# Kernel tuning notes

Measured on AMD Instinct MI355X. Metric: run time of the kernel, lower is better.

Reference implementation:

```python
import math
import jax, jax.numpy as jnp
import numpy as np

WH, WW = 8, 8
NUM_HEADS = 4
EMBED_DIMS = 128
N_TOK = WH * WW

# --- static relative position index (N, N) ---
_coords = np.stack(np.meshgrid(np.arange(WH), np.arange(WW), indexing='ij')).reshape(2, -1)
_rel = (_coords[:, :, None] - _coords[:, None, :]).transpose(1, 2, 0).copy()
_rel[..., 0] += WH - 1
_rel[..., 1] += WW - 1
_rel[..., 0] *= 2 * WW - 1
REL_INDEX = _rel.sum(-1)  # (N, N) ints in [0, (2Wh-1)(2Ww-1))

# --- static log-spaced relative coords table ((2Wh-1)*(2Ww-1), 2) ---
_ch = np.arange(-(WH - 1), WH, dtype=np.float32)
_cw = np.arange(-(WW - 1), WW, dtype=np.float32)
_tab = np.stack(np.meshgrid(_ch, _cw, indexing='ij')).reshape(2, -1).T.copy()
_tab[:, 0] /= WH - 1
_tab[:, 1] /= WW - 1
_tab *= 8
COORDS_TABLE = np.sign(_tab) * np.log2(np.abs(_tab) + 1.0) / math.log2(8)  # (225, 2)


def setup_inputs() -> dict:
    key = jax.random.key(0)
    ks = jax.random.split(key, 8)
    B_ = 8192
    C = EMBED_DIMS
    H = NUM_HEADS
    return {
        'x': jax.random.normal(ks[0], (B_, N_TOK, C), dtype=jnp.float32),
        'mask': jnp.zeros((256, N_TOK, N_TOK), dtype=jnp.float32),
        'qkv_w': jax.random.normal(ks[1], (3 * C, C), dtype=jnp.float32) * 0.02,
        'q_bias': jnp.zeros((C,), dtype=jnp.float32),
        'v_bias': jnp.zeros((C,), dtype=jnp.float32),
        'logit_scale': jnp.full((H, 1, 1), math.log(10.0), dtype=jnp.float32),
        'cpb_w1': jax.random.normal(ks[2], (512, 2), dtype=jnp.float32) * 0.02,
        'cpb_b1': jnp.zeros((512,), dtype=jnp.float32),
        'cpb_w2': jax.random.normal(ks[3], (H, 512), dtype=jnp.float32) * 0.02,
        'proj_w': jax.random.normal(ks[4], (C, C), dtype=jnp.float32) * 0.02,
        'proj_b': jnp.zeros((C,), dtype=jnp.float32),
    }


def reference(x, mask, qkv_w, q_bias, v_bias, logit_scale, cpb_w1, cpb_b1, cpb_w2, proj_w, proj_b):
    B_, N, C = x.shape
    H = NUM_HEADS
    D = C // H
    # qkv with q/v bias only (k bias is zero)
    qkv_b = jnp.concatenate([q_bias, jnp.zeros_like(v_bias), v_bias])
    qkv = x @ qkv_w.T + qkv_b                           # (B_, N, 3C)
    qkv = qkv.reshape(B_, N, 3, H, D).transpose(2, 0, 3, 1, 4)
    q, k, v = qkv[0], qkv[1], qkv[2]                    # (B_, H, N, D)
    # cosine attention
    qn = q / jnp.clip(jnp.linalg.norm(q, axis=-1, keepdims=True), 1e-12)
    kn = k / jnp.clip(jnp.linalg.norm(k, axis=-1, keepdims=True), 1e-12)
    attn = jnp.einsum('bhnd,bhmd->bhnm', qn, kn)
    scale = jnp.exp(jnp.minimum(logit_scale, math.log(1.0 / 0.01)))  # (H,1,1)
    attn = attn * scale
    # log-CPB relative position bias
    table = jnp.asarray(COORDS_TABLE, dtype=x.dtype)     # (225, 2)
    hdn = jax.nn.relu(table @ cpb_w1.T + cpb_b1)         # (225, 512)
    bias_table = hdn @ cpb_w2.T                          # (225, H)
    rel_idx = jnp.asarray(REL_INDEX.reshape(-1))
    bias = bias_table[rel_idx].reshape(N, N, H).transpose(2, 0, 1)
    bias = 16.0 * jax.nn.sigmoid(bias)                   # (H, N, N)
    attn = attn + bias[None]
    # shifted-window mask
    nW = mask.shape[0]
    attn = attn.reshape(B_ // nW, nW, H, N, N) + mask[None, :, None]
    attn = jax.nn.softmax(attn.reshape(B_, H, N, N), axis=-1)
    out = jnp.einsum('bhnm,bhmd->bhnd', attn, v)
    out = out.transpose(0, 2, 1, 3).reshape(B_, N, C)
    return out @ proj_w.T + proj_b
```

## Files before the change

### kernel.cpp

```cpp
#include <hip/hip_runtime.h>

typedef __attribute__((ext_vector_type(8))) __bf16 bf16x8;
typedef __attribute__((ext_vector_type(4))) float floatx4;

#define WS_BIAS  131072
#define WS_SCALE 196608
#define WS_TBL   196640
#define WS_ETAB  262144

static __device__ __forceinline__ unsigned short f2bf_u(float f) {
  union { __bf16 b; unsigned short u; } cv; cv.b = (__bf16)f; return cv.u;
}
static __device__ __forceinline__ unsigned pkbf(float lo, float hi) {
  union { __bf16 b[2]; unsigned u; } cv; cv.b[0] = (__bf16)lo; cv.b[1] = (__bf16)hi; return cv.u;
}
static __device__ __forceinline__ float bfu_lo(unsigned u) { return __uint_as_float(u << 16); }
static __device__ __forceinline__ float bfu_hi(unsigned u) { return __uint_as_float(u & 0xffff0000u); }

__global__ void k_prep_weights(const float* __restrict__ qkv_w,
                               const float* __restrict__ proj_w,
                               const float* __restrict__ logit_scale,
                               unsigned short* __restrict__ wsQ,
                               float* __restrict__ wsScale)
{
  int t = blockIdx.x * 256 + threadIdx.x;
  int i4 = t * 4;
  float4 v;
  if (i4 < 49152) v = *reinterpret_cast<const float4*>(qkv_w + i4);
  else            v = *reinterpret_cast<const float4*>(proj_w + (i4 - 49152));
  ushort4 pk;
  pk.x = f2bf_u(v.x); pk.y = f2bf_u(v.y); pk.z = f2bf_u(v.z); pk.w = f2bf_u(v.w);
  *reinterpret_cast<ushort4*>(wsQ + i4) = pk;
  if (t < 4) wsScale[t] = expf(fminf(logit_scale[t], 4.6051702f));
}

__global__ void k_cpb_table(const float* __restrict__ w1, const float* __restrict__ b1,
                            const float* __restrict__ w2, float* __restrict__ tbl)
{
  __shared__ float red[256][4];
  int t = blockIdx.x;
  int i = t / 15, j = t % 15;
  float c0 = 8.f * (float)(i - 7) / 7.f;
  float c1 = 8.f * (float)(j - 7) / 7.f;
  c0 = copysignf(log2f(fabsf(c0) + 1.f) / 3.f, c0);
  c1 = copysignf(log2f(fabsf(c1) + 1.f) / 3.f, c1);
  float a0 = 0.f, a1 = 0.f, a2 = 0.f, a3 = 0.f;
  for (int k = threadIdx.x; k < 512; k += 256) {
    float hd = fmaxf(c0 * w1[2*k] + c1 * w1[2*k+1] + b1[k], 0.f);
    a0 += hd * w2[k]; a1 += hd * w2[512+k]; a2 += hd * w2[1024+k]; a3 += hd * w2[1536+k];
  }
  red[threadIdx.x][0]=a0; red[threadIdx.x][1]=a1; red[threadIdx.x][2]=a2; red[threadIdx.x][3]=a3;
  __syncthreads();
  for (int s = 128; s > 0; s >>= 1) {
    if (threadIdx.x < (unsigned)s) {
      red[threadIdx.x][0] += red[threadIdx.x+s][0];
      red[threadIdx.x][1] += red[threadIdx.x+s][1];
      red[threadIdx.x][2] += red[threadIdx.x+s][2];
      red[threadIdx.x][3] += red[threadIdx.x+s][3];
    }
    __syncthreads();
  }
  if (threadIdx.x < 4) tbl[t*4 + threadIdx.x] = red[0][threadIdx.x];
}

__global__ void k_cpb_bias(const float* __restrict__ tbl, float* __restrict__ biasT)
{
  int idx = blockIdx.x * 256 + threadIdx.x;
  int hh = idx >> 12, n = (idx >> 6) & 63, m = idx & 63;
  int rel = ((n >> 3) - (m >> 3) + 7) * 15 + ((n & 7) - (m & 7) + 7);
  float bv = tbl[rel * 4 + hh];
  biasT[idx] = 16.f / (1.f + expf(-bv));
}

__global__ void k_exp_table(const float* __restrict__ biasT, const float* __restrict__ mask,
                            unsigned short* __restrict__ E)
{
  int idx4 = (blockIdx.x * 256 + threadIdx.x) * 4;
  int wm  = idx4 >> 14;
  int rem = idx4 & 16383;
  int hh  = rem >> 12;
  int nm  = rem & 4095;
  float4 mv = *reinterpret_cast<const float4*>(mask + (wm << 12) + nm);
  float4 bv = *reinterpret_cast<const float4*>(biasT + (hh << 12) + nm);
  ushort4 o;
  o.x = f2bf_u(expf(bv.x + mv.x));
  o.y = f2bf_u(expf(bv.y + mv.y));
  o.z = f2bf_u(expf(bv.z + mv.z));
  o.w = f2bf_u(expf(bv.w + mv.w));
  *reinterpret_cast<ushort4*>(E + idx4) = o;
}

__global__ __launch_bounds__(256, 2) void k_wmsa(
    const float* __restrict__ x,
    const unsigned short* __restrict__ wqkv, const unsigned short* __restrict__ wproj,
    const float* __restrict__ q_bias, const float* __restrict__ v_bias,
    const unsigned short* __restrict__ Etab, const float* __restrict__ scale4,
    const float* __restrict__ proj_b, float* __restrict__ out)
{
  __shared__ char s_x[64 * 256];
  __shared__ char s_qk[4][8192];
  __shared__ char s_vT[4][4096];

  const int blk  = blockIdx.x;
  const int tid  = threadIdx.x;
  const int lane = tid & 63;
  const int h    = tid >> 6;
  const int l15  = lane & 15;
  const int lh   = lane >> 4;
  const int swq  = ((l15 ^ (l15 >> 2)) & 3) << 4;
  const int swp  = (l15 & 7) << 4;
  const floatx4 zf4 = {0.f, 0.f, 0.f, 0.f};

  bf16x8 wvf[4][2], wff[4][4];
  #pragma unroll
  for (int kk = 0; kk < 4; ++kk) {
    #pragma unroll
    for (int ft = 0; ft < 2; ++ft)
      wvf[kk][ft] = *reinterpret_cast<const bf16x8*>(
          wqkv + (size_t)(256 + h * 32 + ft * 16 + l15) * 128 + kk * 32 + lh * 8);
    #pragma unroll
    for (int ff = 0; ff < 4; ++ff) {
      int fb = (ff < 2) ? (h * 32 + ff * 16) : (128 + h * 32 + (ff - 2) * 16);
      wff[kk][ff] = *reinterpret_cast<const bf16x8*>(
          wqkv + (size_t)(fb + l15) * 128 + kk * 32 + lh * 8);
    }
  }
  floatx4 qb0 = *reinterpret_cast<const floatx4*>(q_bias + h * 32 + lh * 4);
  floatx4 qb1 = *reinterpret_cast<const floatx4*>(q_bias + h * 32 + 16 + lh * 4);
  const float vb0 = v_bias[h * 32 + l15], vb1 = v_bias[h * 32 + 16 + l15];
  const float sc  = scale4[h] * 1.44269504f;
  const unsigned short* Eh = Etab + ((size_t)((blk & 255) * 4 + h)) * 4096;

  float4 xpre[8];

  #pragma unroll
  for (int wi = 0; wi < 2; ++wi) {
    const size_t b = (size_t)blk + (size_t)wi * 4096;

    if (wi) __syncthreads();

    {
      int r = tid >> 2;
      if (wi == 0) {
        const float* xb = x + b * 8192;
        #pragma unroll
        for (int cc = 0; cc < 8; ++cc) {
          int c = (tid & 3) + cc * 4;
          float4 v = reinterpret_cast<const float4*>(xb)[r * 32 + c];
          uint2 w; w.x = pkbf(v.x, v.y); w.y = pkbf(v.z, v.w);
          *reinterpret_cast<uint2*>(s_x + r * 256 + ((c * 8) ^ ((r & 7) << 4))) = w;
        }
      } else {
        #pragma unroll
        for (int cc = 0; cc < 8; ++cc) {
          int c = (tid & 3) + cc * 4;
          uint2 w; w.x = pkbf(xpre[cc].x, xpre[cc].y); w.y = pkbf(xpre[cc].z, xpre[cc].w);
          *reinterpret_cast<uint2*>(s_x + r * 256 + ((c * 8) ^ ((r & 7) << 4))) = w;
        }
      }
    }
    __syncthreads();

    floatx4 vacc[4][2];
    floatx4 qk[4][4];
    #pragma unroll
    for (int mt = 0; mt < 4; ++mt) { vacc[mt][0] = zf4; vacc[mt][1] = zf4; }
    #pragma unroll
    for (int ff = 0; ff < 4; ++ff)
      #pragma unroll
      for (int tt = 0; tt < 4; ++tt) qk[ff][tt] = zf4;

    #pragma unroll
    for (int kk = 0; kk < 4; ++kk) {
      bf16x8 xf[4];
      #pragma unroll
      for (int tt = 0; tt < 4; ++tt) {
        int row = tt * 16 + l15;
        xf[tt] = *reinterpret_cast<const bf16x8*>(
            s_x + row * 256 + (((kk * 32 + lh * 8) * 2) ^ ((row & 7) << 4)));
      }
      #pragma unroll
      for (int ft = 0; ft < 2; ++ft)
        #pragma unroll
        for (int mt = 0; mt < 4; ++mt)
          vacc[mt][ft] = __builtin_amdgcn_mfma_f32_16x16x32_bf16(xf[mt], wvf[kk][ft], vacc[mt][ft], 0, 0, 0);
      #pragma unroll
      for (int ff = 0; ff < 4; ++ff)
        #pragma unroll
        for (int tt = 0; tt < 4; ++tt)
          qk[ff][tt] = __builtin_amdgcn_mfma_f32_16x16x32_bf16(wff[kk][ff], xf[tt], qk[ff][tt], 0, 0, 0);
    }

    {
      char* sv = s_vT[h];
      #pragma unroll
      for (int mt = 0; mt < 4; ++mt) {
        #pragma unroll
        for (int ft = 0; ft < 2; ++ft) {
          float vb = ft ? vb1 : vb0;
          int d = ft * 16 + l15;
          uint2 w;
          w.x = pkbf(vacc[mt][ft][0] + vb, vacc[mt][ft][1] + vb);
          w.y = pkbf(vacc[mt][ft][2] + vb, vacc[mt][ft][3] + vb);
          *reinterpret_cast<uint2*>(sv + d * 128 + (((mt * 16 + lh * 4) * 2) ^ swp)) = w;
        }
      }
    }

    #pragma unroll
    for (int tt = 0; tt < 4; ++tt)
      #pragma unroll
      for (int r = 0; r < 4; ++r) { qk[0][tt][r] += qb0[r]; qk[1][tt][r] += qb1[r]; }
    #pragma unroll
    for (int tt = 0; tt < 4; ++tt) {
      float sq = 0.f, sk = 0.f;
      #pragma unroll
      for (int r = 0; r < 4; ++r) {
        sq += qk[0][tt][r] * qk[0][tt][r] + qk[1][tt][r] * qk[1][tt][r];
        sk += qk[2][tt][r] * qk[2][tt][r] + qk[3][tt][r] * qk[3][tt][r];
      }
      sq += __shfl_xor(sq, 16); sq += __shfl_xor(sq, 32);
      sk += __shfl_xor(sk, 16); sk += __shfl_xor(sk, 32);
      float rq = sc  / fmaxf(sqrtf(sq), 1e-12f);
      float rk = 1.f / fmaxf(sqrtf(sk), 1e-12f);
      #pragma unroll
      for (int r = 0; r < 4; ++r) {
        qk[0][tt][r] *= rq; qk[1][tt][r] *= rq;
        qk[2][tt][r] *= rk; qk[3][tt][r] *= rk;
      }
    }

    uint2 e[4][4];
    #pragma unroll
    for (int tn = 0; tn < 4; ++tn)
      #pragma unroll
      for (int tm = 0; tm < 4; ++tm)
        e[tn][tm] = *reinterpret_cast<const uint2*>(
            Eh + (tn * 16 + l15) * 64 + tm * 16 + lh * 4);

    {
      char* sq = s_qk[h];
      #pragma unroll
      for (int tt = 0; tt < 4; ++tt) {
        int row = 16 * tt + l15;
        #pragma unroll
        for (int ff = 0; ff < 2; ++ff) {
          uint2 wq_, wk_;
          wq_.x = pkbf(qk[ff][tt][0],     qk[ff][tt][1]);
          wq_.y = pkbf(qk[ff][tt][2],     qk[ff][tt][3]);
          wk_.x = pkbf(qk[2 + ff][tt][0], qk[2 + ff][tt][1]);
          wk_.y = pkbf(qk[2 + ff][tt][2], qk[2 + ff][tt][3]);
          int colb = (ff * 32 + lh * 8) ^ swq;
          *reinterpret_cast<uint2*>(sq + row * 64 + colb)        = wq_;
          *reinterpret_cast<uint2*>(sq + 4096 + row * 64 + colb) = wk_;
        }
      }
    }

    floatx4 rs;
    {
      const char* sq = s_qk[h];
      bf16x8 qf[4], kf[4];
      #pragma unroll
      for (int tt = 0; tt < 4; ++tt) {
        int row = 16 * tt + l15;
        qf[tt] = *reinterpret_cast<const bf16x8*>(sq + row * 64 + ((lh * 16) ^ swq));
        kf[tt] = *reinterpret_cast<const bf16x8*>(sq + 4096 + row * 64 + ((lh * 16) ^ swq));
      }
      char* sp = s_qk[h];

      #pragma unroll
      for (int tn = 0; tn < 4; ++tn) {
        floatx4 sacc[4];
        #pragma unroll
        for (int tm = 0; tm < 4; ++tm)
          sacc[tm] = __builtin_amdgcn_mfma_f32_16x16x32_bf16(kf[tm], qf[tn], zf4, 0, 0, 0);
        float sum = 0.f;
        uint2 pw[4];
        #pragma unroll
        for (int tm = 0; tm < 4; ++tm) {
          uint2 eu = e[tn][tm];
          float e0 = exp2f(sacc[tm][0]) * bfu_lo(eu.x);
          float e1 = exp2f(sacc[tm][1]) * bfu_hi(eu.x);
          float e2 = exp2f(sacc[tm][2]) * bfu_lo(eu.y);
          float e3 = exp2f(sacc[tm][3]) * bfu_hi(eu.y);
          sum += (e0 + e1) + (e2 + e3);
          pw[tm].x = pkbf(e0, e1); pw[tm].y = pkbf(e2, e3);
        }
        sum += __shfl_xor(sum, 16); sum += __shfl_xor(sum, 32);
        rs[tn] = 1.f / sum;
        int prow = 16 * tn + l15;
        #pragma unroll
        for (int tm = 0; tm < 4; ++tm)
          *reinterpret_cast<uint2*>(sp + prow * 128 + ((tm * 32 + lh * 8) ^ swp)) = pw[tm];
      }
    }

    bf16x8 wp[4][2];
    #pragma unroll
    for (int kk = 0; kk < 4; ++kk)
      #pragma unroll
      for (int ft = 0; ft < 2; ++ft)
        wp[kk][ft] = *reinterpret_cast<const bf16x8*>(
            wproj + (size_t)(h * 32 + ft * 16 + l15) * 128 + kk * 32 + lh * 8);
    if (wi == 0) {
      const float* xb1 = x + ((size_t)blk + 4096) * 8192;
      int r = tid >> 2;
      #pragma unroll
      for (int cc = 0; cc < 8; ++cc) {
        int c = (tid & 3) + cc * 4;
        xpre[cc] = reinterpret_cast<const float4*>(xb1)[r * 32 + c];
      }
    }

    floatx4 oacc[2][4];
    #pragma unroll
    for (int dt = 0; dt < 2; ++dt)
      #pragma unroll
      for (int nt = 0; nt < 4; ++nt) oacc[dt][nt] = zf4;
    {
      const char* sv = s_vT[h];
      const char* sp = s_qk[h];
      #pragma unroll
      for (int kk = 0; kk < 2; ++kk) {
        bf16x8 vf[2];
        #pragma unroll
        for (int dt = 0; dt < 2; ++dt)
          vf[dt] = *reinterpret_cast<const bf16x8*>(
              sv + (dt * 16 + l15) * 128 + ((kk * 64 + lh * 16) ^ swp));
        #pragma unroll
        for (int nt = 0; nt < 4; ++nt) {
          bf16x8 pf = *reinterpret_cast<const bf16x8*>(
              sp + (nt * 16 + l15) * 128 + ((kk * 64 + lh * 16) ^ swp));
          #pragma unroll
          for (int dt = 0; dt < 2; ++dt)
            oacc[dt][nt] = __builtin_amdgcn_mfma_f32_16x16x32_bf16(vf[dt], pf, oacc[dt][nt], 0, 0, 0);
        }
      }
    }
    __syncthreads();

    #pragma unroll
    for (int dt = 0; dt < 2; ++dt) {
      #pragma unroll
      for (int nt = 0; nt < 4; ++nt) {
        int n = nt * 16 + l15;
        uint2 w;
        w.x = pkbf(oacc[dt][nt][0] * rs[nt], oacc[dt][nt][1] * rs[nt]);
        w.y = pkbf(oacc[dt][nt][2] * rs[nt], oacc[dt][nt][3] * rs[nt]);
        *reinterpret_cast<uint2*>(
            s_x + n * 256 + (((h * 32 + dt * 16 + lh * 4) * 2) ^ ((n & 7) << 4))) = w;
      }
    }
    __syncthreads();

    floatx4 pacc[4][2];
    #pragma unroll
    for (int mt = 0; mt < 4; ++mt) { pacc[mt][0] = zf4; pacc[mt][1] = zf4; }
    #pragma unroll
    for (int kk = 0; kk < 4; ++kk) {
      bf16x8 of[4];
      #pragma unroll
      for (int mt = 0; mt < 4; ++mt) {
        int row = mt * 16 + l15;
        of[mt] = *reinterpret_cast<const bf16x8*>(
            s_x + row * 256 + (((kk * 32 + lh * 8) * 2) ^ ((row & 7) << 4)));
      }
      #pragma unroll
      for (int ft = 0; ft < 2; ++ft)
        #pragma unroll
        for (int mt = 0; mt < 4; ++mt)
          pacc[mt][ft] = __builtin_amdgcn_mfma_f32_16x16x32_bf16(of[mt], wp[kk][ft], pacc[mt][ft], 0, 0, 0);
    }
    {
      float pb0 = proj_b[h * 32 + l15], pb1 = proj_b[h * 32 + 16 + l15];
      float* ob = out + b * 8192;
      #pragma unroll
      for (int mt = 0; mt < 4; ++mt)
        #pragma unroll
        for (int r = 0; r < 4; ++r) {
          int n = mt * 16 + lh * 4 + r;
          ob[n * 128 + h * 32 + l15]      = pacc[mt][0][r] + pb0;
          ob[n * 128 + h * 32 + 16 + l15] = pacc[mt][1][r] + pb1;
        }
    }
  }
}

extern "C" void kernel_launch(void* const* d_in, const int* in_sizes, int n_in,
                              void* d_out, int out_size, void* d_ws, size_t ws_size,
                              hipStream_t stream)
{
  const float* x    = (const float*)d_in[0];
  const float* mask = (const float*)d_in[1];
  const float* qkvw = (const float*)d_in[2];
  const float* qb   = (const float*)d_in[3];
  const float* vb   = (const float*)d_in[4];
  const float* ls   = (const float*)d_in[5];
  const float* w1   = (const float*)d_in[6];
  const float* b1   = (const float*)d_in[7];
  const float* w2   = (const float*)d_in[8];
  const float* pw   = (const float*)d_in[9];
  const float* pb   = (const float*)d_in[10];
  float* out = (float*)d_out;
  char* ws = (char*)d_ws;

  unsigned short* wsQ = (unsigned short*)ws;
  float* wsBias  = (float*)(ws + WS_BIAS);
  float* wsScale = (float*)(ws + WS_SCALE);
  float* wsTbl   = (float*)(ws + WS_TBL);
  unsigned short* wsE = (unsigned short*)(ws + WS_ETAB);

  hipLaunchKernelGGL(k_prep_weights, dim3(64), dim3(256), 0, stream, qkvw, pw, ls, wsQ, wsScale);
  hipLaunchKernelGGL(k_cpb_table, dim3(225), dim3(256), 0, stream, w1, b1, w2, wsTbl);
  hipLaunchKernelGGL(k_cpb_bias, dim3(64), dim3(256), 0, stream, wsTbl, wsBias);
  hipLaunchKernelGGL(k_exp_table, dim3(4096), dim3(256), 0, stream, wsBias, mask, wsE);
  hipLaunchKernelGGL(k_wmsa, dim3(4096), dim3(256), 0, stream, x,
                     wsQ, wsQ + 49152, qb, vb, wsE, wsScale, pb, out);
}
```

Before: 289.6 us.

## Split QKV projection into phased V/Q/K passes to cut register pressure

The kernel no longer holds all QKV weight fragments in registers for both windows. It reloads V, Q and K weights from global memory in separate phases, computing each projection and normalizing it before moving on. The software prefetch of the second window's x is dropped, and the exp-bias table is loaded once before the window loop. The aim is to lower live VGPR count and raise occupancy, at the cost of reloading weights each window, reading the x tile from LDS three times, and losing the prefetch overlap.

```diff
diff --git a/kernel.cpp b/kernel.cpp
--- a/kernel.cpp
+++ b/kernel.cpp
@@ -111,27 +111,20 @@
   const int swp  = (l15 & 7) << 4;
   const floatx4 zf4 = {0.f, 0.f, 0.f, 0.f};
 
-  bf16x8 wvf[4][2], wff[4][4];
-  #pragma unroll
-  for (int kk = 0; kk < 4; ++kk) {
-    #pragma unroll
-    for (int ft = 0; ft < 2; ++ft)
-      wvf[kk][ft] = *reinterpret_cast<const bf16x8*>(
-          wqkv + (size_t)(256 + h * 32 + ft * 16 + l15) * 128 + kk * 32 + lh * 8);
-    #pragma unroll
-    for (int ff = 0; ff < 4; ++ff) {
-      int fb = (ff < 2) ? (h * 32 + ff * 16) : (128 + h * 32 + (ff - 2) * 16);
-      wff[kk][ff] = *reinterpret_cast<const bf16x8*>(
-          wqkv + (size_t)(fb + l15) * 128 + kk * 32 + lh * 8);
-    }
-  }
   floatx4 qb0 = *reinterpret_cast<const floatx4*>(q_bias + h * 32 + lh * 4);
   floatx4 qb1 = *reinterpret_cast<const floatx4*>(q_bias + h * 32 + 16 + lh * 4);
   const float vb0 = v_bias[h * 32 + l15], vb1 = v_bias[h * 32 + 16 + l15];
   const float sc  = scale4[h] * 1.44269504f;
+  const float pb0 = proj_b[h * 32 + l15], pb1 = proj_b[h * 32 + 16 + l15];
   const unsigned short* Eh = Etab + ((size_t)((blk & 255) * 4 + h)) * 4096;
 
-  float4 xpre[8];
+  uint2 e[4][4];
+  #pragma unroll
+  for (int tn = 0; tn < 4; ++tn)
+    #pragma unroll
+    for (int tm = 0; tm < 4; ++tm)
+      e[tn][tm] = *reinterpret_cast<const uint2*>(
+          Eh + (tn * 16 + l15) * 64 + tm * 16 + lh * 4);
 
   #pragma unroll
   for (int wi = 0; wi < 2; ++wi) {
@@ -140,58 +133,44 @@
     if (wi) __syncthreads();
 
     {
+      const float* xb = x + b * 8192;
       int r = tid >> 2;
-      if (wi == 0) {
-        const float* xb = x + b * 8192;
-        #pragma unroll
-        for (int cc = 0; cc < 8; ++cc) {
-          int c = (tid & 3) + cc * 4;
-          float4 v = reinterpret_cast<const float4*>(xb)[r * 32 + c];
-          uint2 w; w.x = pkbf(v.x, v.y); w.y = pkbf(v.z, v.w);
-          *reinterpret_cast<uint2*>(s_x + r * 256 + ((c * 8) ^ ((r & 7) << 4))) = w;
-        }
-      } else {
-        #pragma unroll
-        for (int cc = 0; cc < 8; ++cc) {
-          int c = (tid & 3) + cc * 4;
-          uint2 w; w.x = pkbf(xpre[cc].x, xpre[cc].y); w.y = pkbf(xpre[cc].z, xpre[cc].w);
-          *reinterpret_cast<uint2*>(s_x + r * 256 + ((c * 8) ^ ((r & 7) << 4))) = w;
-        }
+      #pragma unroll
+      for (int cc = 0; cc < 8; ++cc) {
+        int c = (tid & 3) + cc * 4;
+        float4 v = reinterpret_cast<const float4*>(xb)[r * 32 + c];
+        uint2 w; w.x = pkbf(v.x, v.y); w.y = pkbf(v.z, v.w);
+        *reinterpret_cast<uint2*>(s_x + r * 256 + ((c * 8) ^ ((r & 7) << 4))) = w;
       }
     }
     __syncthreads();
 
-    floatx4 vacc[4][2];
-    floatx4 qk[4][4];
-    #pragma unroll
-    for (int mt = 0; mt < 4; ++mt) { vacc[mt][0] = zf4; vacc[mt][1] = zf4; }
-    #pragma unroll
-    for (int ff = 0; ff < 4; ++ff)
-      #pragma unroll
-      for (int tt = 0; tt < 4; ++tt) qk[ff][tt] = zf4;
-
-    #pragma unroll
-    for (int kk = 0; kk < 4; ++kk) {
-      bf16x8 xf[4];
-      #pragma unroll
-      for (int tt = 0; tt < 4; ++tt) {
-        int row = tt * 16 + l15;
-        xf[tt] = *reinterpret_cast<const bf16x8*>(
-            s_x + row * 256 + (((kk * 32 + lh * 8) * 2) ^ ((row & 7) << 4)));
-      }
-      #pragma unroll
-      for (int ft = 0; ft < 2; ++ft)
-        #pragma unroll
-        for (int mt = 0; mt < 4; ++mt)
-          vacc[mt][ft] = __builtin_amdgcn_mfma_f32_16x16x32_bf16(xf[mt], wvf[kk][ft], vacc[mt][ft], 0, 0, 0);
-      #pragma unroll
-      for (int ff = 0; ff < 4; ++ff)
-        #pragma unroll
-        for (int tt = 0; tt < 4; ++tt)
-          qk[ff][tt] = __builtin_amdgcn_mfma_f32_16x16x32_bf16(wff[kk][ff], xf[tt], qk[ff][tt], 0, 0, 0);
-    }
-
-    {
+    {
+      bf16x8 wv[4][2];
+      #pragma unroll
+      for (int kk = 0; kk < 4; ++kk)
+        #pragma unroll
+        for (int ft = 0; ft < 2; ++ft)
+          wv[kk][ft] = *reinterpret_cast<const bf16x8*>(
+              wqkv + (size_t)(256 + h * 32 + ft * 16 + l15) * 128 + kk * 32 + lh * 8);
+      floatx4 vacc[4][2];
+      #pragma unroll
+      for (int mt = 0; mt < 4; ++mt) { vacc[mt][0] = zf4; vacc[mt][1] = zf4; }
+      #pragma unroll
+      for (int kk = 0; kk < 4; ++kk) {
+        bf16x8 xf[4];
+        #pragma unroll
+        for (int tt = 0; tt < 4; ++tt) {
+          int row = tt * 16 + l15;
+          xf[tt] = *reinterpret_cast<const bf16x8*>(
+              s_x + row * 256 + (((kk * 32 + lh * 8) * 2) ^ ((row & 7) << 4)));
+        }
+        #pragma unroll
+        for (int ft = 0; ft < 2; ++ft)
+          #pragma unroll
+          for (int mt = 0; mt < 4; ++mt)
+            vacc[mt][ft] = __builtin_amdgcn_mfma_f32_16x16x32_bf16(xf[mt], wv[kk][ft], vacc[mt][ft], 0, 0, 0);
+      }
       char* sv = s_vT[h];
       #pragma unroll
       for (int mt = 0; mt < 4; ++mt) {
@@ -207,68 +186,125 @@
       }
     }
 
-    #pragma unroll
-    for (int tt = 0; tt < 4; ++tt)
-      #pragma unroll
-      for (int r = 0; r < 4; ++r) { qk[0][tt][r] += qb0[r]; qk[1][tt][r] += qb1[r]; }
-    #pragma unroll
-    for (int tt = 0; tt < 4; ++tt) {
-      float sq = 0.f, sk = 0.f;
-      #pragma unroll
-      for (int r = 0; r < 4; ++r) {
-        sq += qk[0][tt][r] * qk[0][tt][r] + qk[1][tt][r] * qk[1][tt][r];
-        sk += qk[2][tt][r] * qk[2][tt][r] + qk[3][tt][r] * qk[3][tt][r];
-      }
-      sq += __shfl_xor(sq, 16); sq += __shfl_xor(sq, 32);
-      sk += __shfl_xor(sk, 16); sk += __shfl_xor(sk, 32);
-      float rq = sc  / fmaxf(sqrtf(sq), 1e-12f);
-      float rk = 1.f / fmaxf(sqrtf(sk), 1e-12f);
-      #pragma unroll
-      for (int r = 0; r < 4; ++r) {
-        qk[0][tt][r] *= rq; qk[1][tt][r] *= rq;
-        qk[2][tt][r] *= rk; qk[3][tt][r] *= rk;
-      }
-    }
-
-    uint2 e[4][4];
-    #pragma unroll
-    for (int tn = 0; tn < 4; ++tn)
-      #pragma unroll
-      for (int tm = 0; tm < 4; ++tm)
-        e[tn][tm] = *reinterpret_cast<const uint2*>(
-            Eh + (tn * 16 + l15) * 64 + tm * 16 + lh * 4);
-
-    {
+    bf16x8 qf[4], kf[4];
+    {
+      bf16x8 wq[4][2];
+      #pragma unroll
+      for (int kk = 0; kk < 4; ++kk)
+        #pragma unroll
+        for (int ft = 0; ft < 2; ++ft)
+          wq[kk][ft] = *reinterpret_cast<const bf16x8*>(
+              wqkv + (size_t)(h * 32 + ft * 16 + l15) * 128 + kk * 32 + lh * 8);
+      floatx4 qacc[2][4];
+      #pragma unroll
+      for (int ff = 0; ff < 2; ++ff)
+        #pragma unroll
+        for (int tt = 0; tt < 4; ++tt) qacc[ff][tt] = zf4;
+      #pragma unroll
+      for (int kk = 0; kk < 4; ++kk) {
+        bf16x8 xf[4];
+        #pragma unroll
+        for (int tt = 0; tt < 4; ++tt) {
+          int row = tt * 16 + l15;
+          xf[tt] = *reinterpret_cast<const bf16x8*>(
+              s_x + row * 256 + (((kk * 32 + lh * 8) * 2) ^ ((row & 7) << 4)));
+        }
+        #pragma unroll
+        for (int ff = 0; ff < 2; ++ff)
+          #pragma unroll
+          for (int tt = 0; tt < 4; ++tt)
+            qacc[ff][tt] = __builtin_amdgcn_mfma_f32_16x16x32_bf16(wq[kk][ff], xf[tt], qacc[ff][tt], 0, 0, 0);
+      }
+      #pragma unroll
+      for (int tt = 0; tt < 4; ++tt) {
+        #pragma unroll
+        for (int r = 0; r < 4; ++r) { qacc[0][tt][r] += qb0[r]; qacc[1][tt][r] += qb1[r]; }
+        float sq = 0.f;
+        #pragma unroll
+        for (int r = 0; r < 4; ++r)
+          sq += qacc[0][tt][r] * qacc[0][tt][r] + qacc[1][tt][r] * qacc[1][tt][r];
+        sq += __shfl_xor(sq, 16); sq += __shfl_xor(sq, 32);
+        float rq = sc / fmaxf(sqrtf(sq), 1e-12f);
+        #pragma unroll
+        for (int r = 0; r < 4; ++r) { qacc[0][tt][r] *= rq; qacc[1][tt][r] *= rq; }
+      }
       char* sq = s_qk[h];
       #pragma unroll
       for (int tt = 0; tt < 4; ++tt) {
         int row = 16 * tt + l15;
         #pragma unroll
         for (int ff = 0; ff < 2; ++ff) {
-          uint2 wq_, wk_;
-          wq_.x = pkbf(qk[ff][tt][0],     qk[ff][tt][1]);
-          wq_.y = pkbf(qk[ff][tt][2],     qk[ff][tt][3]);
-          wk_.x = pkbf(qk[2 + ff][tt][0], qk[2 + ff][tt][1]);
-          wk_.y = pkbf(qk[2 + ff][tt][2], qk[2 + ff][tt][3]);
-          int colb = (ff * 32 + lh * 8) ^ swq;
-          *reinterpret_cast<uint2*>(sq + row * 64 + colb)        = wq_;
-          *reinterpret_cast<uint2*>(sq + 4096 + row * 64 + colb) = wk_;
-        }
-      }
-    }
-
-    floatx4 rs;
-    {
-      const char* sq = s_qk[h];
-      bf16x8 qf[4], kf[4];
+          uint2 w;
+          w.x = pkbf(qacc[ff][tt][0], qacc[ff][tt][1]);
+          w.y = pkbf(qacc[ff][tt][2], qacc[ff][tt][3]);
+          *reinterpret_cast<uint2*>(sq + row * 64 + ((ff * 32 + lh * 8) ^ swq)) = w;
+        }
+      }
+      #pragma unroll
+      for (int tt = 0; tt < 4; ++tt)
+        qf[tt] = *reinterpret_cast<const bf16x8*>(sq + (16 * tt + l15) * 64 + ((lh * 16) ^ swq));
+    }
+
+    {
+      bf16x8 wk[4][2];
+      #pragma unroll
+      for (int kk = 0; kk < 4; ++kk)
+        #pragma unroll
+        for (int ft = 0; ft < 2; ++ft)
+          wk[kk][ft] = *reinterpret_cast<const bf16x8*>(
+              wqkv + (size_t)(128 + h * 32 + ft * 16 + l15) * 128 + kk * 32 + lh * 8);
+      floatx4 kacc[2][4];
+      #pragma unroll
+      for (int ff = 0; ff < 2; ++ff)
+        #pragma unroll
+        for (int tt = 0; tt < 4; ++tt) kacc[ff][tt] = zf4;
+      #pragma unroll
+      for (int kk = 0; kk < 4; ++kk) {
+        bf16x8 xf[4];
+        #pragma unroll
+        for (int tt = 0; tt < 4; ++tt) {
+          int row = tt * 16 + l15;
+          xf[tt] = *reinterpret_cast<const bf16x8*>(
+              s_x + row * 256 + (((kk * 32 + lh * 8) * 2) ^ ((row & 7) << 4)));
+        }
+        #pragma unroll
+        for (int ff = 0; ff < 2; ++ff)
+          #pragma unroll
+          for (int tt = 0; tt < 4; ++tt)
+            kacc[ff][tt] = __builtin_amdgcn_mfma_f32_16x16x32_bf16(wk[kk][ff], xf[tt], kacc[ff][tt], 0, 0, 0);
+      }
+      #pragma unroll
+      for (int tt = 0; tt < 4; ++tt) {
+        float sk = 0.f;
+        #pragma unroll
+        for (int r = 0; r < 4; ++r)
+          sk += kacc[0][tt][r] * kacc[0][tt][r] + kacc[1][tt][r] * kacc[1][tt][r];
+        sk += __shfl_xor(sk, 16); sk += __shfl_xor(sk, 32);
+        float rk = 1.f / fmaxf(sqrtf(sk), 1e-12f);
+        #pragma unroll
+        for (int r = 0; r < 4; ++r) { kacc[0][tt][r] *= rk; kacc[1][tt][r] *= rk; }
+      }
+      char* sq = s_qk[h];
       #pragma unroll
       for (int tt = 0; tt < 4; ++tt) {
         int row = 16 * tt + l15;
-        qf[tt] = *reinterpret_cast<const bf16x8*>(sq + row * 64 + ((lh * 16) ^ swq));
-        kf[tt] = *reinterpret_cast<const bf16x8*>(sq + 4096 + row * 64 + ((lh * 16) ^ swq));
-      }
+        #pragma unroll
+        for (int ff = 0; ff < 2; ++ff) {
+          uint2 w;
+          w.x = pkbf(kacc[ff][tt][0], kacc[ff][tt][1]);
+          w.y = pkbf(kacc[ff][tt][2], kacc[ff][tt][3]);
+          *reinterpret_cast<uint2*>(sq + 4096 + row * 64 + ((ff * 32 + lh * 8) ^ swq)) = w;
+        }
+      }
+      #pragma unroll
+      for (int tt = 0; tt < 4; ++tt)
+        kf[tt] = *reinterpret_cast<const bf16x8*>(
+            sq + 4096 + (16 * tt + l15) * 64 + ((lh * 16) ^ swq));
+    }
+
+    floatx4 rs;
+    {
       char* sp = s_qk[h];
-
       #pragma unroll
       for (int tn = 0; tn < 4; ++tn) {
         floatx4 sacc[4];
@@ -296,23 +332,6 @@
       }
     }
 
-    bf16x8 wp[4][2];
-    #pragma unroll
-    for (int kk = 0; kk < 4; ++kk)
-      #pragma unroll
-      for (int ft = 0; ft < 2; ++ft)
-        wp[kk][ft] = *reinterpret_cast<const bf16x8*>(
-            wproj + (size_t)(h * 32 + ft * 16 + l15) * 128 + kk * 32 + lh * 8);
-    if (wi == 0) {
-      const float* xb1 = x + ((size_t)blk + 4096) * 8192;
-      int r = tid >> 2;
-      #pragma unroll
-      for (int cc = 0; cc < 8; ++cc) {
-        int c = (tid & 3) + cc * 4;
-        xpre[cc] = reinterpret_cast<const float4*>(xb1)[r * 32 + c];
-      }
-    }
-
     floatx4 oacc[2][4];
     #pragma unroll
     for (int dt = 0; dt < 2; ++dt)
@@ -354,26 +373,32 @@
     }
     __syncthreads();
 
-    floatx4 pacc[4][2];
-    #pragma unroll
-    for (int mt = 0; mt < 4; ++mt) { pacc[mt][0] = zf4; pacc[mt][1] = zf4; }
-    #pragma unroll
-    for (int kk = 0; kk < 4; ++kk) {
-      bf16x8 of[4];
-      #pragma unroll
-      for (int mt = 0; mt < 4; ++mt) {
-        int row = mt * 16 + l15;
-        of[mt] = *reinterpret_cast<const bf16x8*>(
-            s_x + row * 256 + (((kk * 32 + lh * 8) * 2) ^ ((row & 7) << 4)));
-      }
-      #pragma unroll
-      for (int ft = 0; ft < 2; ++ft)
-        #pragma unroll
-        for (int mt = 0; mt < 4; ++mt)
-          pacc[mt][ft] = __builtin_amdgcn_mfma_f32_16x16x32_bf16(of[mt], wp[kk][ft], pacc[mt][ft], 0, 0, 0);
-    }
-    {
-      float pb0 = proj_b[h * 32 + l15], pb1 = proj_b[h * 32 + 16 + l15];
+    {
+      bf16x8 wp[4][2];
+      #pragma unroll
+      for (int kk = 0; kk < 4; ++kk)
+        #pragma unroll
+        for (int ft = 0; ft < 2; ++ft)
+          wp[kk][ft] = *reinterpret_cast<const bf16x8*>(
+              wproj + (size_t)(h * 32 + ft * 16 + l15) * 128 + kk * 32 + lh * 8);
+      floatx4 pacc[4][2];
+      #pragma unroll
+      for (int mt = 0; mt < 4; ++mt) { pacc[mt][0] = zf4; pacc[mt][1] = zf4; }
+      #pragma unroll
+      for (int kk = 0; kk < 4; ++kk) {
+        bf16x8 of[4];
+        #pragma unroll
+        for (int mt = 0; mt < 4; ++mt) {
+          int row = mt * 16 + l15;
+          of[mt] = *reinterpret_cast<const bf16x8*>(
+              s_x + row * 256 + (((kk * 32 + lh * 8) * 2) ^ ((row & 7) << 4)));
+        }
+        #pragma unroll
+        for (int ft = 0; ft < 2; ++ft)
+          #pragma unroll
+          for (int mt = 0; mt < 4; ++mt)
+            pacc[mt][ft] = __builtin_amdgcn_mfma_f32_16x16x32_bf16(of[mt], wp[kk][ft], pacc[mt][ft], 0, 0, 0);
+      }
       float* ob = out + b * 8192;
       #pragma unroll
       for (int mt = 0; mt < 4; ++mt)
```

After: 248.6 us, median of 4. -14.2%, faster.
